# Kernel tuning notes

Hardware: AMD Instinct MI355X
Metric: run time of the kernel (lower is better)

The kernel has to match this reference:

```python
import jax, jax.numpy as jnp
import numpy as np

H = 4096        # hidden_size
NH = 32         # num query heads
NKV = 8         # num kv heads
D = H // NH     # head_dim = 128
S = 2048        # num tokens (single causal sequence)
THETA = 1000000.0
SCALE = D ** -0.5


def _rope(x, positions):
    # neox-style (rotate-half) RoPE over full head_dim, as vLLM's get_rope default
    half = D // 2
    inv_freq = 1.0 / (THETA ** (jnp.arange(half, dtype=jnp.float32) / half))
    ang = positions.astype(jnp.float32)[:, None] * inv_freq          # [S, D/2]
    cos = jnp.cos(ang)[:, None, :]                                   # [S, 1, D/2]
    sin = jnp.sin(ang)[:, None, :]
    x1, x2 = x[..., :half], x[..., half:]
    return jnp.concatenate([x1 * cos - x2 * sin, x2 * cos + x1 * sin], axis=-1)


def setup_inputs() -> dict:
    key = jax.random.key(0)
    k1, k2, k3 = jax.random.split(key, 3)
    positions = jnp.arange(S, dtype=jnp.int32)
    hidden_states = jax.random.normal(k1, (S, H), dtype=jnp.float32)
    w_qkv = jax.random.normal(k2, ((NH + 2 * NKV) * D, H), dtype=jnp.float32) * 0.02
    w_o = jax.random.normal(k3, (H, NH * D), dtype=jnp.float32) * 0.02
    return {"positions": positions, "hidden_states": hidden_states,
            "w_qkv": w_qkv, "w_o": w_o}


def reference(positions, hidden_states, w_qkv, w_o):
    # fused QKV projection (Linear, bias=False): x @ W^T
    qkv = hidden_states @ w_qkv.T                                    # [S, (NH+2*NKV)*D]
    q, k, v = jnp.split(qkv, [NH * D, (NH + NKV) * D], axis=-1)
    q = q.reshape(S, NH, D)
    k = k.reshape(S, NKV, D)
    v = v.reshape(S, NKV, D)
    # RoPE on q and k
    q = _rope(q, positions)
    k = _rope(k, positions)
    # GQA causal attention: group NH query heads onto NKV kv heads
    g = NH // NKV
    qg = q.reshape(S, NKV, g, D)
    scores = jnp.einsum('qhgd,khd->hgqk', qg, k) * SCALE             # [NKV, g, S, S]
    causal = positions[:, None] >= positions[None, :]                # [S, S]
    scores = jnp.where(causal[None, None], scores, jnp.float32(-1e30))
    probs = jax.nn.softmax(scores, axis=-1)
    o = jnp.einsum('hgqk,khd->qhgd', probs, v).reshape(S, NH * D)
    return o @ w_o.T                                                 # [S, H]
```

## Files before the change

### kernel.cpp

```cpp
#include <hip/hip_runtime.h>
#include <hip/hip_bf16.h>

#define S_LEN 2048
#define HID 4096
#define NH 32
#define NKV 8
#define DH 128
#define QKV_N ((NH + 2 * NKV) * DH)
#define SCALE_ATT 0.08838834764831845f

typedef __bf16 bf16;
typedef __bf16 bf16x8 __attribute__((ext_vector_type(8)));
typedef float f32x4 __attribute__((ext_vector_type(4)));

__device__ inline f32x4 mfma16(bf16x8 a, bf16x8 b, f32x4 c) {
    return __builtin_amdgcn_mfma_f32_16x16x32_bf16(a, b, c, 0, 0, 0);
}

__device__ inline bf16x8 load8(const float* p) {
    const float4 a = ((const float4*)p)[0];
    const float4 b = ((const float4*)p)[1];
    bf16x8 r;
    r[0] = (bf16)a.x; r[1] = (bf16)a.y; r[2] = (bf16)a.z; r[3] = (bf16)a.w;
    r[4] = (bf16)b.x; r[5] = (bf16)b.y; r[6] = (bf16)b.z; r[7] = (bf16)b.w;
    return r;
}
__device__ inline bf16x8 load8(const bf16* p) { return *(const bf16x8*)p; }

__device__ inline void load_lds16(const bf16* g, bf16* lds_base) {
    __builtin_amdgcn_global_load_lds(
        (const __attribute__((address_space(1))) void*)g,
        (__attribute__((address_space(3))) void*)lds_base, 16, 0, 0);
}

__global__ __launch_bounds__(256) void cvt_kernel(const float* __restrict__ src,
                                                  bf16* __restrict__ dst, int n8) {
    int i = blockIdx.x * 256 + threadIdx.x;
    if (i >= n8) return;
    *(bf16x8*)&dst[(size_t)i * 8] = load8(&src[(size_t)i * 8]);
}

template <typename OutT>
__global__ __launch_bounds__(256) void gemm_bt_swz(const bf16* __restrict__ A,
                                                   const bf16* __restrict__ B,
                                                   OutT* __restrict__ C,
                                                   int K, int lda, int ldc) {
    const int tid = threadIdx.x;
    const int lane = tid & 63;
    const int w = tid >> 6;
    const int m0 = blockIdx.y * 128;
    const int n0 = blockIdx.x * 128;
    const int wm = (w >> 1) * 64;
    const int wn = (w & 1) * 64;
    const int ln = lane & 15;
    const int qo = lane >> 4;

    __shared__ bf16 As[128 * 64];
    __shared__ bf16 Bs[128 * 64];

    const int rseg = lane >> 3;
    const int gc = (lane & 7) ^ (rseg & 7);

    f32x4 acc[4][4];
#pragma unroll
    for (int mi = 0; mi < 4; ++mi)
#pragma unroll
        for (int ni = 0; ni < 4; ++ni) acc[mi][ni] = f32x4{0.f, 0.f, 0.f, 0.f};

    for (int k0 = 0; k0 < K; k0 += 64) {
#pragma unroll
        for (int j = 0; j < 4; ++j) {
            const int seg = w * 4 + j;
            const int r = seg * 8 + rseg;
            load_lds16(&A[(size_t)(m0 + r) * lda + k0 + gc * 8], &As[seg * 512]);
            load_lds16(&B[(size_t)(n0 + r) * K + k0 + gc * 8], &Bs[seg * 512]);
        }
        __syncthreads();
#pragma unroll
        for (int kk = 0; kk < 2; ++kk) {
            bf16x8 af[4], bfr[4];
#pragma unroll
            for (int mi = 0; mi < 4; ++mi) {
                const int m = wm + mi * 16 + ln;
                const int sc = (kk * 4 + qo) ^ (ln & 7);
                af[mi] = *(const bf16x8*)&As[m * 64 + sc * 8];
            }
#pragma unroll
            for (int ni = 0; ni < 4; ++ni) {
                const int n = wn + ni * 16 + ln;
                const int sc = (kk * 4 + qo) ^ (ln & 7);
                bfr[ni] = *(const bf16x8*)&Bs[n * 64 + sc * 8];
            }
#pragma unroll
            for (int mi = 0; mi < 4; ++mi)
#pragma unroll
                for (int ni = 0; ni < 4; ++ni)
                    acc[mi][ni] = mfma16(af[mi], bfr[ni], acc[mi][ni]);
        }
        __syncthreads();
    }
#pragma unroll
    for (int mi = 0; mi < 4; ++mi)
#pragma unroll
        for (int ni = 0; ni < 4; ++ni)
#pragma unroll
            for (int r = 0; r < 4; ++r) {
                int row = m0 + wm + mi * 16 + qo * 4 + r;
                int col = n0 + wn + ni * 16 + ln;
                C[(size_t)row * ldc + col] = (OutT)acc[mi][ni][r];
            }
}

template <typename AT, typename OutT>
__global__ __launch_bounds__(256) void gemm_bt(const AT* __restrict__ A,
                                               const float* __restrict__ B,
                                               OutT* __restrict__ C,
                                               int K, int lda, int ldc) {
    const int tid = threadIdx.x;
    const int lane = tid & 63;
    const int w = tid >> 6;
    const int m0 = blockIdx.y * 128;
    const int n0 = blockIdx.x * 128;
    const int wm = (w >> 1) * 64;
    const int wn = (w & 1) * 64;
    const int ln = lane & 15;
    const int qo = lane >> 4;

    __shared__ bf16 As[128 * 72];
    __shared__ bf16 Bs[128 * 72];

    f32x4 acc[4][4];
#pragma unroll
    for (int mi = 0; mi < 4; ++mi)
#pragma unroll
        for (int ni = 0; ni < 4; ++ni) acc[mi][ni] = f32x4{0.f, 0.f, 0.f, 0.f};

    for (int k0 = 0; k0 < K; k0 += 64) {
#pragma unroll
        for (int i = 0; i < 4; ++i) {
            int v = tid + i * 256;
            int row = v >> 3;
            int col = (v & 7) * 8;
            *(bf16x8*)&As[row * 72 + col] = load8(&A[(size_t)(m0 + row) * lda + k0 + col]);
            *(bf16x8*)&Bs[row * 72 + col] = load8(&B[(size_t)(n0 + row) * K + k0 + col]);
        }
        __syncthreads();
#pragma unroll
        for (int kk = 0; kk < 64; kk += 32) {
            bf16x8 af[4], bfr[4];
#pragma unroll
            for (int mi = 0; mi < 4; ++mi)
                af[mi] = *(const bf16x8*)&As[(wm + mi * 16 + ln) * 72 + kk + qo * 8];
#pragma unroll
            for (int ni = 0; ni < 4; ++ni)
                bfr[ni] = *(const bf16x8*)&Bs[(wn + ni * 16 + ln) * 72 + kk + qo * 8];
#pragma unroll
            for (int mi = 0; mi < 4; ++mi)
#pragma unroll
                for (int ni = 0; ni < 4; ++ni)
                    acc[mi][ni] = mfma16(af[mi], bfr[ni], acc[mi][ni]);
        }
        __syncthreads();
    }
#pragma unroll
    for (int mi = 0; mi < 4; ++mi)
#pragma unroll
        for (int ni = 0; ni < 4; ++ni)
#pragma unroll
            for (int r = 0; r < 4; ++r) {
                int row = m0 + wm + mi * 16 + qo * 4 + r;
                int col = n0 + wn + ni * 16 + ln;
                C[(size_t)row * ldc + col] = (OutT)acc[mi][ni][r];
            }
}

__global__ __launch_bounds__(256) void rope_kernel(bf16* __restrict__ qkv,
                                                   const int* __restrict__ positions) {
    int idx = blockIdx.x * 256 + threadIdx.x;
    const int total = S_LEN * (NH + NKV) * 64;
    if (idx >= total) return;
    int d = idx & 63;
    int t = idx >> 6;
    int head = t % (NH + NKV);
    int s = t / (NH + NKV);
    size_t base = (size_t)s * QKV_N + (head < NH ? head * DH : NH * DH + (head - NH) * DH);
    float x1 = (float)qkv[base + d];
    float x2 = (float)qkv[base + d + 64];
    float pos = (float)positions[s];
    float inv = expf(-0.21586735246819178f * (float)d);
    float ang = pos * inv;
    float c = cosf(ang);
    float sn = sinf(ang);
    qkv[base + d] = (bf16)(x1 * c - x2 * sn);
    qkv[base + d + 64] = (bf16)(x2 * c + x1 * sn);
}

__global__ __launch_bounds__(256) void vtrans_kernel(const bf16* __restrict__ qkv,
                                                     bf16* __restrict__ vt_g) {
    const int tid = threadIdx.x;
    const int s0 = blockIdx.x * 64;
    const int kvh = blockIdx.y;
    __shared__ bf16 Ls[64 * 136];
#pragma unroll
    for (int i = 0; i < 4; ++i) {
        int v = tid + i * 256;
        int row = v >> 4;
        int col = (v & 15) * 8;
        *(bf16x8*)&Ls[row * 136 + col] =
            *(const bf16x8*)&qkv[(size_t)(s0 + row) * QKV_N + (NH + NKV) * DH + kvh * DH + col];
    }
    __syncthreads();
#pragma unroll
    for (int i = 0; i < 4; ++i) {
        int u = tid + i * 256;
        int d = u >> 3;
        int sg = (u & 7) * 8;
        bf16x8 r;
#pragma unroll
        for (int j = 0; j < 8; ++j) r[j] = Ls[(sg + j) * 136 + d];
        *(bf16x8*)&vt_g[((size_t)kvh * DH + d) * S_LEN + s0 + sg] = r;
    }
}

__global__ __launch_bounds__(256) void attn_kernel(bf16* __restrict__ qkv,
                                                   const bf16* __restrict__ vt_g) {
    const int tid = threadIdx.x;
    const int lane = tid & 63;
    const int w = tid >> 6;
    const int ln = lane & 15;
    const int qo = lane >> 4;
    const int qtile = (int)gridDim.x - 1 - (int)blockIdx.x;
    const int hq = blockIdx.y;
    const int kvh = hq >> 2;
    const int q0 = qtile * 64;

    __shared__ __align__(16) char smem_raw[2 * 17408 + 18432];
    bf16* Qs = (bf16*)smem_raw;
    bf16* Ps = (bf16*)smem_raw;
    bf16* Ks = (bf16*)(smem_raw + 17408);
    bf16* Vt = (bf16*)(smem_raw + 2 * 17408);

#pragma unroll
    for (int i = 0; i < 4; ++i) {
        int v = tid + i * 256;
        int row = v >> 4;
        int col = (v & 15) * 8;
        *(bf16x8*)&Qs[row * 136 + col] =
            *(const bf16x8*)&qkv[(size_t)(q0 + row) * QKV_N + hq * DH + col];
    }
    __syncthreads();

    bf16x8 aq[4];
#pragma unroll
    for (int ko = 0; ko < 4; ++ko)
        aq[ko] = *(const bf16x8*)&Qs[(w * 16 + ln) * 136 + ko * 32 + qo * 8];

    f32x4 acc[8];
#pragma unroll
    for (int n = 0; n < 8; ++n) acc[n] = f32x4{0.f, 0.f, 0.f, 0.f};
    float m_r[4], l_r[4];
#pragma unroll
    for (int r = 0; r < 4; ++r) { m_r[r] = -1e30f; l_r[r] = 0.f; }

    bf16* Ps_w = &Ps[w * 16 * 72];
    const bf16* vsrc = vt_g + (size_t)kvh * DH * S_LEN;

    for (int kt = 0; kt <= qtile; ++kt) {
        const int k0 = kt * 64;
#pragma unroll
        for (int i = 0; i < 4; ++i) {
            int v = tid + i * 256;
            int row = v >> 4;
            int col = (v & 15) * 8;
            *(bf16x8*)&Ks[row * 136 + col] =
                *(const bf16x8*)&qkv[(size_t)(k0 + row) * QKV_N + NH * DH + kvh * DH + col];
        }
#pragma unroll
        for (int i = 0; i < 4; ++i) {
            int u = tid + i * 256;
            int d = u >> 3;
            int kc = (u & 7) * 8;
            *(bf16x8*)&Vt[d * 72 + kc] =
                *(const bf16x8*)&vsrc[(size_t)d * S_LEN + k0 + kc];
        }
        __syncthreads();

        float p[4][4];
#pragma unroll
        for (int ni = 0; ni < 4; ++ni) {
            f32x4 sacc = f32x4{0.f, 0.f, 0.f, 0.f};
#pragma unroll
            for (int ko = 0; ko < 4; ++ko) {
                bf16x8 bk = *(const bf16x8*)&Ks[(ni * 16 + ln) * 136 + ko * 32 + qo * 8];
                sacc = mfma16(aq[ko], bk, sacc);
            }
#pragma unroll
            for (int r = 0; r < 4; ++r) {
                float val = sacc[r] * SCALE_ATT;
                int qrow = q0 + w * 16 + qo * 4 + r;
                int kcol = k0 + ni * 16 + ln;
                if (kcol > qrow) val = -1e30f;
                p[ni][r] = val;
            }
        }
        float alpha[4];
#pragma unroll
        for (int r = 0; r < 4; ++r) {
            float mx = fmaxf(fmaxf(p[0][r], p[1][r]), fmaxf(p[2][r], p[3][r]));
#pragma unroll
            for (int off = 1; off < 16; off <<= 1)
                mx = fmaxf(mx, __shfl_xor(mx, off, 64));
            float mnew = fmaxf(m_r[r], mx);
            alpha[r] = __expf(m_r[r] - mnew);
            float rs = 0.f;
#pragma unroll
            for (int ni = 0; ni < 4; ++ni) {
                float e = __expf(p[ni][r] - mnew);
                p[ni][r] = e;
                rs += e;
            }
#pragma unroll
            for (int off = 1; off < 16; off <<= 1) rs += __shfl_xor(rs, off, 64);
            l_r[r] = l_r[r] * alpha[r] + rs;
            m_r[r] = mnew;
        }
#pragma unroll
        for (int n = 0; n < 8; ++n)
#pragma unroll
            for (int r = 0; r < 4; ++r) acc[n][r] *= alpha[r];
#pragma unroll
        for (int ni = 0; ni < 4; ++ni)
#pragma unroll
            for (int r = 0; r < 4; ++r)
                Ps_w[(qo * 4 + r) * 72 + ni * 16 + ln] = (bf16)p[ni][r];
        __syncthreads();
#pragma unroll
        for (int ko2 = 0; ko2 < 2; ++ko2) {
            bf16x8 pf = *(const bf16x8*)&Ps_w[ln * 72 + ko2 * 32 + qo * 8];
#pragma unroll
            for (int n = 0; n < 8; ++n) {
                bf16x8 vf = *(const bf16x8*)&Vt[(n * 16 + ln) * 72 + ko2 * 32 + qo * 8];
                acc[n] = mfma16(pf, vf, acc[n]);
            }
        }
        __syncthreads();
    }
#pragma unroll
    for (int r = 0; r < 4; ++r) {
        float invl = 1.f / l_r[r];
        int qrow = q0 + w * 16 + qo * 4 + r;
#pragma unroll
        for (int n = 0; n < 8; ++n)
            qkv[(size_t)qrow * QKV_N + hq * DH + n * 16 + ln] = (bf16)(acc[n][r] * invl);
    }
}

extern "C" void kernel_launch(void* const* d_in, const int* in_sizes, int n_in,
                              void* d_out, int out_size, void* d_ws, size_t ws_size,
                              hipStream_t stream) {
    const int* positions = (const int*)d_in[0];
    const float* hidden = (const float*)d_in[1];
    const float* w_qkv = (const float*)d_in[2];
    const float* w_o = (const float*)d_in[3];
    float* out = (float*)d_out;

    const size_t n_qkv = (size_t)S_LEN * QKV_N;
    const size_t n_vt = (size_t)NKV * DH * S_LEN;
    const size_t n_hid = (size_t)S_LEN * HID;
    const size_t n_wqkv = (size_t)QKV_N * HID;
    const size_t n_wo = (size_t)HID * HID;

    const size_t need_min = (n_qkv + n_vt) * sizeof(bf16);
    const size_t need_full = (n_qkv + n_vt + n_hid + n_wqkv + n_wo) * sizeof(bf16);
    if (ws_size < need_min) return;

    bf16* qkv = (bf16*)d_ws;
    bf16* vt_g = qkv + n_qkv;
    bf16* hid_b = vt_g + n_vt;
    bf16* wqkv_b = hid_b + n_hid;
    bf16* wo_b = wqkv_b + n_wqkv;
    const bool full = ws_size >= need_full;

    if (full) {
        cvt_kernel<<<(int)(n_hid / 8 + 255) / 256, 256, 0, stream>>>(hidden, hid_b, (int)(n_hid / 8));
        cvt_kernel<<<(int)(n_wqkv / 8 + 255) / 256, 256, 0, stream>>>(w_qkv, wqkv_b, (int)(n_wqkv / 8));
        cvt_kernel<<<(int)(n_wo / 8 + 255) / 256, 256, 0, stream>>>(w_o, wo_b, (int)(n_wo / 8));
        gemm_bt_swz<<<dim3(QKV_N / 128, S_LEN / 128), 256, 0, stream>>>(hid_b, wqkv_b, qkv, HID, HID, QKV_N);
    } else {
        gemm_bt<<<dim3(QKV_N / 128, S_LEN / 128), 256, 0, stream>>>(hidden, w_qkv, qkv, HID, HID, QKV_N);
    }
    const int total = S_LEN * (NH + NKV) * 64;
    rope_kernel<<<(total + 255) / 256, 256, 0, stream>>>(qkv, positions);
    vtrans_kernel<<<dim3(S_LEN / 64, NKV), 256, 0, stream>>>(qkv, vt_g);
    attn_kernel<<<dim3(S_LEN / 64, NH), 256, 0, stream>>>(qkv, vt_g);
    if (full) {
        gemm_bt_swz<<<dim3(HID / 128, S_LEN / 128), 256, 0, stream>>>(qkv, wo_b, out, HID, QKV_N, HID);
    } else {
        gemm_bt<<<dim3(HID / 128, S_LEN / 128), 256, 0, stream>>>(qkv, w_o, out, HID, QKV_N, HID);
    }
}
```

Baseline: 609.2 us.

## Rewrite attention with 32x32 MFMA, async double-buffered LDS, and register-resident P

Rewrites the attention kernel so each block covers 128 queries, with each wave owning 32 rows via 32x32x16 bf16 MFMA. K and V^T tiles are double-buffered in LDS through asynchronous global_load_lds with an XOR swizzle, so the next tile loads while the current one is computed. P is kept in registers via lane shuffles instead of a round trip through LDS, and softmax uses exp2 with a prescaled log2e factor. The grid is reordered head-major and waves skip fully masked tiles. In exchange, register pressure is higher and occupancy may drop.

```diff
diff --git a/kernel.cpp b/kernel.cpp
--- a/kernel.cpp
+++ b/kernel.cpp
@@ -8,13 +8,19 @@
 #define DH 128
 #define QKV_N ((NH + 2 * NKV) * DH)
 #define SCALE_ATT 0.08838834764831845f
+#define SCALE2_ATT 0.12751744f
 
 typedef __bf16 bf16;
 typedef __bf16 bf16x8 __attribute__((ext_vector_type(8)));
+typedef __bf16 bf16x4 __attribute__((ext_vector_type(4)));
 typedef float f32x4 __attribute__((ext_vector_type(4)));
+typedef float f32x16 __attribute__((ext_vector_type(16)));
 
 __device__ inline f32x4 mfma16(bf16x8 a, bf16x8 b, f32x4 c) {
     return __builtin_amdgcn_mfma_f32_16x16x32_bf16(a, b, c, 0, 0, 0);
+}
+__device__ inline f32x16 mfma32(bf16x8 a, bf16x8 b, f32x16 c) {
+    return __builtin_amdgcn_mfma_f32_32x32x16_bf16(a, b, c, 0, 0, 0);
 }
 
 __device__ inline bf16x8 load8(const float* p) {
@@ -31,6 +37,13 @@
     __builtin_amdgcn_global_load_lds(
         (const __attribute__((address_space(1))) void*)g,
         (__attribute__((address_space(3))) void*)lds_base, 16, 0, 0);
+}
+
+__device__ inline unsigned pack2_bf16(float lo, float hi) {
+    union { bf16 h[2]; unsigned u; } r;
+    r.h[0] = (bf16)lo;
+    r.h[1] = (bf16)hi;
+    return r.u;
 }
 
 __global__ __launch_bounds__(256) void cvt_kernel(const float* __restrict__ src,
@@ -227,132 +240,161 @@
     const int tid = threadIdx.x;
     const int lane = tid & 63;
     const int w = tid >> 6;
-    const int ln = lane & 15;
-    const int qo = lane >> 4;
-    const int qtile = (int)gridDim.x - 1 - (int)blockIdx.x;
-    const int hq = blockIdx.y;
+    const int ln = lane & 31;
+    const int hi = lane >> 5;
+    const int hq = blockIdx.x;
+    const int qtile = (int)gridDim.y - 1 - (int)blockIdx.y;
     const int kvh = hq >> 2;
-    const int q0 = qtile * 64;
-
-    __shared__ __align__(16) char smem_raw[2 * 17408 + 18432];
-    bf16* Qs = (bf16*)smem_raw;
-    bf16* Ps = (bf16*)smem_raw;
-    bf16* Ks = (bf16*)(smem_raw + 17408);
-    bf16* Vt = (bf16*)(smem_raw + 2 * 17408);
-
-#pragma unroll
-    for (int i = 0; i < 4; ++i) {
-        int v = tid + i * 256;
-        int row = v >> 4;
-        int col = (v & 15) * 8;
-        *(bf16x8*)&Qs[row * 136 + col] =
-            *(const bf16x8*)&qkv[(size_t)(q0 + row) * QKV_N + hq * DH + col];
-    }
+    const int q0 = qtile * 128;
+    const int qrow = q0 + w * 32 + ln;
+
+    __shared__ __align__(128) bf16 Ks[2][64 * 128];
+    __shared__ __align__(128) bf16 Vt[2][128 * 64];
+
+    bf16x8 qf[8];
+    {
+        const bf16* qptr = qkv + (size_t)qrow * QKV_N + hq * DH + hi * 8;
+#pragma unroll
+        for (int s = 0; s < 8; ++s) qf[s] = *(const bf16x8*)(qptr + s * 16);
+    }
+
+    const bf16* ksrc = qkv + NH * DH + kvh * DH;
+    const bf16* vsrc = vt_g + (size_t)kvh * DH * S_LEN;
+    const int kcK = lane & 15;
+    const int krs = lane >> 4;
+    const int kcV = lane & 7;
+    const int vrs = lane >> 3;
+
+    auto stage = [&](int buf, int kt) {
+        const int k0s = kt * 64;
+#pragma unroll
+        for (int j = 0; j < 4; ++j) {
+            int r = w * 16 + j * 4 + krs;
+            load_lds16(ksrc + (size_t)(k0s + r) * QKV_N + ((kcK ^ (r & 7)) * 8),
+                       &Ks[buf][(w * 16 + j * 4) * 128]);
+        }
+#pragma unroll
+        for (int j = 0; j < 4; ++j) {
+            int d = w * 32 + j * 8 + vrs;
+            load_lds16(vsrc + (size_t)d * S_LEN + k0s + ((kcV ^ (d & 7)) * 8),
+                       &Vt[buf][(w * 32 + j * 8) * 64]);
+        }
+    };
+
+    f32x16 acc[4];
+#pragma unroll
+    for (int t = 0; t < 4; ++t)
+#pragma unroll
+        for (int r = 0; r < 16; ++r) acc[t][r] = 0.f;
+    float m2 = -1e30f, l = 0.f;
+
+    const int kt_last = (q0 + 127) >> 6;
+    int buf = 0;
+    stage(0, 0);
     __syncthreads();
 
-    bf16x8 aq[4];
-#pragma unroll
-    for (int ko = 0; ko < 4; ++ko)
-        aq[ko] = *(const bf16x8*)&Qs[(w * 16 + ln) * 136 + ko * 32 + qo * 8];
-
-    f32x4 acc[8];
-#pragma unroll
-    for (int n = 0; n < 8; ++n) acc[n] = f32x4{0.f, 0.f, 0.f, 0.f};
-    float m_r[4], l_r[4];
-#pragma unroll
-    for (int r = 0; r < 4; ++r) { m_r[r] = -1e30f; l_r[r] = 0.f; }
-
-    bf16* Ps_w = &Ps[w * 16 * 72];
-    const bf16* vsrc = vt_g + (size_t)kvh * DH * S_LEN;
-
-    for (int kt = 0; kt <= qtile; ++kt) {
+    for (int kt = 0; kt <= kt_last; ++kt) {
+        if (kt < kt_last) stage(buf ^ 1, kt + 1);
         const int k0 = kt * 64;
-#pragma unroll
-        for (int i = 0; i < 4; ++i) {
-            int v = tid + i * 256;
-            int row = v >> 4;
-            int col = (v & 15) * 8;
-            *(bf16x8*)&Ks[row * 136 + col] =
-                *(const bf16x8*)&qkv[(size_t)(k0 + row) * QKV_N + NH * DH + kvh * DH + col];
-        }
-#pragma unroll
-        for (int i = 0; i < 4; ++i) {
-            int u = tid + i * 256;
-            int d = u >> 3;
-            int kc = (u & 7) * 8;
-            *(bf16x8*)&Vt[d * 72 + kc] =
-                *(const bf16x8*)&vsrc[(size_t)d * S_LEN + k0 + kc];
+        if (k0 <= q0 + w * 32 + 31) {
+            f32x16 st[2];
+#pragma unroll
+            for (int t = 0; t < 2; ++t)
+#pragma unroll
+                for (int r = 0; r < 16; ++r) st[t][r] = 0.f;
+            const bf16* Kb = &Ks[buf][0];
+            __builtin_amdgcn_s_setprio(1);
+#pragma unroll
+            for (int t = 0; t < 2; ++t) {
+                const int key = t * 32 + ln;
+#pragma unroll
+                for (int s = 0; s < 8; ++s) {
+                    bf16x8 kf =
+                        *(const bf16x8*)&Kb[key * 128 + (((2 * s + hi) ^ (key & 7)) * 8)];
+                    st[t] = mfma32(kf, qf[s], st[t]);
+                }
+            }
+            __builtin_amdgcn_s_setprio(0);
+            const bool needMask = (k0 + 63 > q0 + w * 32);
+            float tmax = -1e30f;
+#pragma unroll
+            for (int t = 0; t < 2; ++t)
+#pragma unroll
+                for (int r = 0; r < 16; ++r) {
+                    int kcol = k0 + t * 32 + (r & 3) + 8 * (r >> 2) + 4 * hi;
+                    float v = st[t][r] * SCALE2_ATT;
+                    if (needMask && kcol > qrow) v = -1e30f;
+                    st[t][r] = v;
+                    tmax = fmaxf(tmax, v);
+                }
+            tmax = fmaxf(tmax, __shfl_xor(tmax, 32, 64));
+            float mnew = fmaxf(m2, tmax);
+            float alpha = exp2f(m2 - mnew);
+            float rs = 0.f;
+#pragma unroll
+            for (int t = 0; t < 2; ++t)
+#pragma unroll
+                for (int r = 0; r < 16; ++r) {
+                    float e = exp2f(st[t][r] - mnew);
+                    st[t][r] = e;
+                    rs += e;
+                }
+            rs += __shfl_xor(rs, 32, 64);
+            l = l * alpha + rs;
+            m2 = mnew;
+#pragma unroll
+            for (int t = 0; t < 4; ++t)
+#pragma unroll
+                for (int r = 0; r < 16; ++r) acc[t][r] *= alpha;
+            unsigned cw[16];
+#pragma unroll
+            for (int i = 0; i < 16; ++i)
+                cw[i] = pack2_bf16(st[i >> 3][2 * (i & 7)], st[i >> 3][2 * (i & 7) + 1]);
+            bf16x8 pa[4];
+#pragma unroll
+            for (int ks = 0; ks < 4; ++ks) {
+                const int base = (ks >> 1) * 8 + (ks & 1) * 4;
+                union { unsigned u[4]; bf16x8 v; } pk;
+#pragma unroll
+                for (int e = 0; e < 2; ++e) {
+                    unsigned A = cw[base + e];
+                    unsigned B = cw[base + 2 + e];
+                    unsigned tA = (unsigned)__shfl_xor((int)A, 32, 64);
+                    unsigned tB = (unsigned)__shfl_xor((int)B, 32, 64);
+                    pk.u[e] = hi ? tB : A;
+                    pk.u[e + 2] = hi ? B : tA;
+                }
+                pa[ks] = pk.v;
+            }
+            const bf16* Vb = &Vt[buf][0];
+            __builtin_amdgcn_s_setprio(1);
+#pragma unroll
+            for (int dt = 0; dt < 4; ++dt) {
+                const int d = dt * 32 + ln;
+#pragma unroll
+                for (int ks = 0; ks < 4; ++ks) {
+                    bf16x8 vf =
+                        *(const bf16x8*)&Vb[d * 64 + (((2 * ks + hi) ^ (d & 7)) * 8)];
+                    acc[dt] = mfma32(vf, pa[ks], acc[dt]);
+                }
+            }
+            __builtin_amdgcn_s_setprio(0);
         }
         __syncthreads();
-
-        float p[4][4];
-#pragma unroll
-        for (int ni = 0; ni < 4; ++ni) {
-            f32x4 sacc = f32x4{0.f, 0.f, 0.f, 0.f};
-#pragma unroll
-            for (int ko = 0; ko < 4; ++ko) {
-                bf16x8 bk = *(const bf16x8*)&Ks[(ni * 16 + ln) * 136 + ko * 32 + qo * 8];
-                sacc = mfma16(aq[ko], bk, sacc);
-            }
-#pragma unroll
-            for (int r = 0; r < 4; ++r) {
-                float val = sacc[r] * SCALE_ATT;
-                int qrow = q0 + w * 16 + qo * 4 + r;
-                int kcol = k0 + ni * 16 + ln;
-                if (kcol > qrow) val = -1e30f;
-                p[ni][r] = val;
-            }
-        }
-        float alpha[4];
-#pragma unroll
-        for (int r = 0; r < 4; ++r) {
-            float mx = fmaxf(fmaxf(p[0][r], p[1][r]), fmaxf(p[2][r], p[3][r]));
-#pragma unroll
-            for (int off = 1; off < 16; off <<= 1)
-                mx = fmaxf(mx, __shfl_xor(mx, off, 64));
-            float mnew = fmaxf(m_r[r], mx);
-            alpha[r] = __expf(m_r[r] - mnew);
-            float rs = 0.f;
-#pragma unroll
-            for (int ni = 0; ni < 4; ++ni) {
-                float e = __expf(p[ni][r] - mnew);
-                p[ni][r] = e;
-                rs += e;
-            }
-#pragma unroll
-            for (int off = 1; off < 16; off <<= 1) rs += __shfl_xor(rs, off, 64);
-            l_r[r] = l_r[r] * alpha[r] + rs;
-            m_r[r] = mnew;
-        }
-#pragma unroll
-        for (int n = 0; n < 8; ++n)
-#pragma unroll
-            for (int r = 0; r < 4; ++r) acc[n][r] *= alpha[r];
-#pragma unroll
-        for (int ni = 0; ni < 4; ++ni)
-#pragma unroll
-            for (int r = 0; r < 4; ++r)
-                Ps_w[(qo * 4 + r) * 72 + ni * 16 + ln] = (bf16)p[ni][r];
-        __syncthreads();
-#pragma unroll
-        for (int ko2 = 0; ko2 < 2; ++ko2) {
-            bf16x8 pf = *(const bf16x8*)&Ps_w[ln * 72 + ko2 * 32 + qo * 8];
-#pragma unroll
-            for (int n = 0; n < 8; ++n) {
-                bf16x8 vf = *(const bf16x8*)&Vt[(n * 16 + ln) * 72 + ko2 * 32 + qo * 8];
-                acc[n] = mfma16(pf, vf, acc[n]);
-            }
-        }
-        __syncthreads();
-    }
-#pragma unroll
-    for (int r = 0; r < 4; ++r) {
-        float invl = 1.f / l_r[r];
-        int qrow = q0 + w * 16 + qo * 4 + r;
-#pragma unroll
-        for (int n = 0; n < 8; ++n)
-            qkv[(size_t)qrow * QKV_N + hq * DH + n * 16 + ln] = (bf16)(acc[n][r] * invl);
-    }
+        buf ^= 1;
+    }
+
+    const float invl = 1.f / l;
+    bf16* outp = qkv + (size_t)qrow * QKV_N + hq * DH;
+#pragma unroll
+    for (int dt = 0; dt < 4; ++dt)
+#pragma unroll
+        for (int rq = 0; rq < 4; ++rq) {
+            bf16x4 o;
+#pragma unroll
+            for (int i = 0; i < 4; ++i) o[i] = (bf16)(acc[dt][rq * 4 + i] * invl);
+            *(bf16x4*)(outp + dt * 32 + rq * 8 + hi * 4) = o;
+        }
 }
 
 extern "C" void kernel_launch(void* const* d_in, const int* in_sizes, int n_in,
@@ -392,7 +434,7 @@
     const int total = S_LEN * (NH + NKV) * 64;
     rope_kernel<<<(total + 255) / 256, 256, 0, stream>>>(qkv, positions);
     vtrans_kernel<<<dim3(S_LEN / 64, NKV), 256, 0, stream>>>(qkv, vt_g);
-    attn_kernel<<<dim3(S_LEN / 64, NH), 256, 0, stream>>>(qkv, vt_g);
+    attn_kernel<<<dim3(NH, S_LEN / 128), 256, 0, stream>>>(qkv, vt_g);
     if (full) {
         gemm_bt_swz<<<dim3(HID / 128, S_LEN / 128), 256, 0, stream>>>(qkv, wo_b, out, HID, QKV_N, HID);
     } else {
```

Result: faster. 551.0 us (-9.6%).
